# Kernel tuning notes

Hardware: AMD Instinct MI355X
Metric: run time of the kernel (lower is better)

The kernel has to match this reference:

```python
import jax, jax.numpy as jnp
import numpy as np

N = 100000   # number of nodes
D = 32       # uniform degree (CSR ptr = arange(N+1)*D)
B = 2048     # query batch size
F_IN, F_H, F_OUT = 64, 128, 64


def setup_inputs() -> dict:
    key = jax.random.key(0)
    ks = jax.random.split(key, 7)
    x = jax.random.normal(ks[0], (N, F_IN), dtype=jnp.float32)
    times = jax.random.uniform(ks[1], (B,), dtype=jnp.float32)
    ts = jax.random.uniform(ks[2], (N * D,), dtype=jnp.float32)
    W0 = jax.random.normal(ks[3], (F_IN, F_H), dtype=jnp.float32) / np.sqrt(F_IN)
    b0 = jnp.zeros((F_H,), dtype=jnp.float32)
    W1 = jax.random.normal(ks[4], (F_H, F_OUT), dtype=jnp.float32) / np.sqrt(F_H)
    b1 = jnp.zeros((F_OUT,), dtype=jnp.float32)
    batch = jax.random.randint(ks[5], (B,), 0, N, dtype=jnp.int64 if jax.config.jax_enable_x64 else jnp.int32)
    idx = jax.random.randint(ks[6], (N * D,), 0, N, dtype=jnp.int64 if jax.config.jax_enable_x64 else jnp.int32)
    return dict(x=x, times=times, ts=ts, W0=W0, b0=b0, W1=W1, b1=b1, batch=batch, idx=idx)


def reference(x, times, ts, W0, b0, W1, b1, batch, idx):
    # CSR with uniform degree D -> dense neighbor/timestamp matrices [N, D]
    idx_m = idx.reshape(N, D)
    ts_m = ts.reshape(N, D)

    # ---- layer-2 frontier: temporal neighbors of each query node + self loop
    nbrs1 = idx_m[batch]                      # [B, D]
    ts1 = ts_m[batch]                         # [B, D]
    mask1 = ts1 <= times[:, None]             # [B, D] edges with ts <= node time
    nodes = jnp.concatenate([nbrs1, batch[:, None]], axis=1)   # [B, D+1] (self appended)
    t2 = jnp.concatenate([ts1, times[:, None]], axis=1)        # [B, D+1] neighbor query times

    # ---- layer-1: for every frontier (node, time), temporal neighbors + self
    nbrs2 = idx_m[nodes]                      # [B, D+1, D]
    ts2 = ts_m[nodes]                         # [B, D+1, D]
    mask2 = ts2 <= t2[..., None]              # [B, D+1, D]

    # layer 0 embeddings are raw features; masked mean == scatter_mean with self loop
    h_nb = x[nbrs2]                           # [B, D+1, D, F_IN]  (dominant gather)
    agg0 = jnp.where(mask2[..., None], h_nb, 0.0).sum(axis=-2) + x[nodes]  # [B, D+1, F_IN]
    cnt0 = (mask2.sum(axis=-1) + 1).astype(x.dtype)[..., None]             # [B, D+1, 1]
    h1 = jax.nn.relu(agg0 / cnt0 @ W0 + b0)   # [B, D+1, F_H] = act(gcns[0](scatter_mean))

    # ---- layer-2 aggregation over (masked neighbors + self)
    mask_full = jnp.concatenate([mask1, jnp.ones((B, 1), dtype=bool)], axis=1)  # [B, D+1]
    agg1 = jnp.where(mask_full[..., None], h1, 0.0).sum(axis=1)                 # [B, F_H]
    cnt1 = mask_full.sum(axis=1).astype(x.dtype)[:, None]                       # [B, 1]
    out = jax.nn.relu(agg1 / cnt1 @ W1 + b1)  # [B, F_OUT] = act(gcns[1](scatter_mean))
    return out
```

## Files before the change

kernel.cpp:

```cpp
#include <hip/hip_runtime.h>

#define DEG   32
#define F_IN  64
#define F_H   128
#define F_OUT 64
#define NW    8
#define BLOCK (NW * 64)

__launch_bounds__(BLOCK, 4)
__global__ void flowgnn_kernel(const float* __restrict__ x,
                               const float* __restrict__ times,
                               const float* __restrict__ ts,
                               const float* __restrict__ W0,
                               const float* __restrict__ b0,
                               const float* __restrict__ W1,
                               const float* __restrict__ b1,
                               const int*   __restrict__ batch,
                               const int*   __restrict__ idx,
                               float*       __restrict__ out)
{
    __shared__ __align__(16) float W0s[F_IN * F_H];
    __shared__ float t2_s[DEG + 1];
    __shared__ int   nodes_s[DEG + 1];
    __shared__ __align__(16) float meanw[NW * F_IN];
    __shared__ __align__(16) float red[NW * F_H];
    __shared__ __align__(16) float aggm[F_H];

    const int b    = blockIdx.x;
    const int t    = threadIdx.x;
    const int wid  = t >> 6;
    const int lane = t & 63;

    const int   node0 = batch[b];
    const float tb    = times[b];

    {
        const float4* src = (const float4*)W0;
        float4*       dst = (float4*)W0s;
        #pragma unroll
        for (int i = t; i < (F_IN * F_H) / 4; i += BLOCK) dst[i] = src[i];
    }
    if (t < DEG) {
        t2_s[t]    = ts [node0 * DEG + t];
        nodes_s[t] = idx[node0 * DEG + t];
    }
    if (t == DEG) {
        t2_s[DEG]    = tb;
        nodes_s[DEG] = node0;
    }
    __syncthreads();

    const float b0x = b0[2 * lane];
    const float b0y = b0[2 * lane + 1];
    float a1x = 0.f, a1y = 0.f;

    for (int j = wid; j <= DEG; j += NW) {
        const float tq = t2_s[j];
        if (!(tq <= tb)) continue;

        const int node = nodes_s[j];
        const int l32  = lane & 31;
        const int   nb = idx[node * DEG + l32];
        const float tn = ts [node * DEG + l32];

        float acc = x[node * F_IN + lane];

        const unsigned long long bal = __ballot(tn <= tq);
        const unsigned ms = __builtin_amdgcn_readfirstlane((unsigned)(bal & 0xffffffffULL));
        const float cntf = (float)(__popc(ms) + 1);

        #pragma unroll
        for (int g = 0; g < 2; ++g) {
            float v[16];
            #pragma unroll
            for (int n = 0; n < 16; ++n) {
                v[n] = 0.f;
                const int r = g * 16 + n;
                if (ms & (1u << r)) {
                    const int nbr = __builtin_amdgcn_readlane(nb, r);
                    v[n] = x[nbr * F_IN + lane];
                }
            }
            #pragma unroll
            for (int n = 0; n < 16; ++n) acc += v[n];
        }
        const float mean = acc / cntf;

        meanw[wid * F_IN + lane] = mean;

        float hx = 0.f, hy = 0.f;
        #pragma unroll
        for (int f4 = 0; f4 < F_IN / 4; ++f4) {
            const float4 m4 = *(const float4*)&meanw[wid * F_IN + 4 * f4];
            const float2 wa = *(const float2*)&W0s[(4 * f4 + 0) * F_H + 2 * lane];
            const float2 wb = *(const float2*)&W0s[(4 * f4 + 1) * F_H + 2 * lane];
            const float2 wc = *(const float2*)&W0s[(4 * f4 + 2) * F_H + 2 * lane];
            const float2 wd = *(const float2*)&W0s[(4 * f4 + 3) * F_H + 2 * lane];
            hx += m4.x * wa.x; hy += m4.x * wa.y;
            hx += m4.y * wb.x; hy += m4.y * wb.y;
            hx += m4.z * wc.x; hy += m4.z * wc.y;
            hx += m4.w * wd.x; hy += m4.w * wd.y;
        }
        a1x += fmaxf(hx + b0x, 0.f);
        a1y += fmaxf(hy + b0y, 0.f);
    }

    red[wid * F_H + 2 * lane]     = a1x;
    red[wid * F_H + 2 * lane + 1] = a1y;
    __syncthreads();

    if (wid == 0) {
        bool mf = false;
        if (lane <= DEG) mf = (t2_s[lane] <= tb);
        const float cnt1 = (float)__popcll(__ballot(mf));

        float sx = 0.f, sy = 0.f;
        #pragma unroll
        for (int w = 0; w < NW; ++w) {
            sx += red[w * F_H + 2 * lane];
            sy += red[w * F_H + 2 * lane + 1];
        }
        aggm[2 * lane]     = sx / cnt1;
        aggm[2 * lane + 1] = sy / cnt1;

        float o = b1[lane];
        #pragma unroll
        for (int k4 = 0; k4 < F_H / 4; ++k4) {
            const float4 a4 = *(const float4*)&aggm[4 * k4];
            o += a4.x * W1[(4 * k4 + 0) * F_OUT + lane];
            o += a4.y * W1[(4 * k4 + 1) * F_OUT + lane];
            o += a4.z * W1[(4 * k4 + 2) * F_OUT + lane];
            o += a4.w * W1[(4 * k4 + 3) * F_OUT + lane];
        }
        out[b * F_OUT + lane] = fmaxf(o, 0.f);
    }
}

extern "C" void kernel_launch(void* const* d_in, const int* in_sizes, int n_in,
                              void* d_out, int out_size, void* d_ws, size_t ws_size,
                              hipStream_t stream)
{
    const float* x     = (const float*)d_in[0];
    const float* times = (const float*)d_in[1];
    const float* ts    = (const float*)d_in[2];
    const float* W0    = (const float*)d_in[3];
    const float* b0    = (const float*)d_in[4];
    const float* W1    = (const float*)d_in[5];
    const float* b1    = (const float*)d_in[6];
    const int*   batch = (const int*)d_in[7];
    const int*   idx   = (const int*)d_in[8];
    float*       out   = (float*)d_out;

    const int B = in_sizes[1];
    flowgnn_kernel<<<B, BLOCK, 0, stream>>>(x, times, ts, W0, b0, W1, b1, batch, idx, out);
}
```

Baseline: 133.5 us.

## Prefetch neighbor indices/masks into LDS and software-pipeline gathers with GEMM

```diff
diff --git a/kernel.cpp b/kernel.cpp
--- a/kernel.cpp
+++ b/kernel.cpp
@@ -7,7 +7,7 @@
 #define NW    8
 #define BLOCK (NW * 64)
 
-__launch_bounds__(BLOCK, 4)
+__launch_bounds__(BLOCK, 6)
 __global__ void flowgnn_kernel(const float* __restrict__ x,
                                const float* __restrict__ times,
                                const float* __restrict__ ts,
@@ -19,20 +19,31 @@
                                const int*   __restrict__ idx,
                                float*       __restrict__ out)
 {
-    __shared__ __align__(16) float W0s[F_IN * F_H];
-    __shared__ float t2_s[DEG + 1];
-    __shared__ int   nodes_s[DEG + 1];
-    __shared__ __align__(16) float meanw[NW * F_IN];
-    __shared__ __align__(16) float red[NW * F_H];
-    __shared__ __align__(16) float aggm[F_H];
+    __shared__ __align__(16) float smem[9868];
+    float*    W0s     = smem;
+    int*      idx_s   = (int*)(smem + 8192);
+    float*    t2_s    = smem + 9248;
+    int*      nodes_s = (int*)(smem + 9284);
+    unsigned* mask_s  = (unsigned*)(smem + 9320);
+    float*    meanw   = smem + 9356;
 
     const int b    = blockIdx.x;
     const int t    = threadIdx.x;
     const int wid  = t >> 6;
     const int lane = t & 63;
+    const int l32  = lane & 31;
+    const int hsel = (lane >> 5) << 4;
 
     const int   node0 = batch[b];
     const float tb    = times[b];
+    const float2* __restrict__ x2 = (const float2*)x;
+
+    if (t < DEG) {
+        t2_s[t]    = ts [node0 * DEG + t];
+        nodes_s[t] = idx[node0 * DEG + t];
+    }
+    if (t == DEG) { t2_s[DEG] = tb; nodes_s[DEG] = node0; }
+    __syncthreads();
 
     {
         const float4* src = (const float4*)W0;
@@ -40,54 +51,34 @@
         #pragma unroll
         for (int i = t; i < (F_IN * F_H) / 4; i += BLOCK) dst[i] = src[i];
     }
-    if (t < DEG) {
-        t2_s[t]    = ts [node0 * DEG + t];
-        nodes_s[t] = idx[node0 * DEG + t];
-    }
-    if (t == DEG) {
-        t2_s[DEG]    = tb;
-        nodes_s[DEG] = node0;
+    #pragma unroll
+    for (int q = 0; q < 3; ++q) {
+        const int p = t + q * BLOCK;
+        bool bit = false;
+        if (p < (DEG + 1) * DEG) {
+            const int j = p >> 5, d = p & 31;
+            const int nd = nodes_s[j];
+            idx_s[p] = idx[nd * DEG + d];
+            bit = (ts[nd * DEG + d] <= t2_s[j]);
+        }
+        const unsigned long long bal = __ballot(bit);
+        const int prow = (q * BLOCK + (t & ~63)) >> 5;
+        if (p < (DEG + 1) * DEG) {
+            if (lane == 0)  mask_s[prow]     = (unsigned)(bal & 0xffffffffULL);
+            if (lane == 32) mask_s[prow + 1] = (unsigned)(bal >> 32);
+        }
     }
     __syncthreads();
+
+    const unsigned long long liveM =
+        __ballot((lane <= DEG) ? (t2_s[lane] <= tb) : false);
 
     const float b0x = b0[2 * lane];
     const float b0y = b0[2 * lane + 1];
     float a1x = 0.f, a1y = 0.f;
+    int jprev = -1;
 
-    for (int j = wid; j <= DEG; j += NW) {
-        const float tq = t2_s[j];
-        if (!(tq <= tb)) continue;
-
-        const int node = nodes_s[j];
-        const int l32  = lane & 31;
-        const int   nb = idx[node * DEG + l32];
-        const float tn = ts [node * DEG + l32];
-
-        float acc = x[node * F_IN + lane];
-
-        const unsigned long long bal = __ballot(tn <= tq);
-        const unsigned ms = __builtin_amdgcn_readfirstlane((unsigned)(bal & 0xffffffffULL));
-        const float cntf = (float)(__popc(ms) + 1);
-
-        #pragma unroll
-        for (int g = 0; g < 2; ++g) {
-            float v[16];
-            #pragma unroll
-            for (int n = 0; n < 16; ++n) {
-                v[n] = 0.f;
-                const int r = g * 16 + n;
-                if (ms & (1u << r)) {
-                    const int nbr = __builtin_amdgcn_readlane(nb, r);
-                    v[n] = x[nbr * F_IN + lane];
-                }
-            }
-            #pragma unroll
-            for (int n = 0; n < 16; ++n) acc += v[n];
-        }
-        const float mean = acc / cntf;
-
-        meanw[wid * F_IN + lane] = mean;
-
+    auto do_gemm1 = [&]() {
         float hx = 0.f, hy = 0.f;
         #pragma unroll
         for (int f4 = 0; f4 < F_IN / 4; ++f4) {
@@ -103,17 +94,51 @@
         }
         a1x += fmaxf(hx + b0x, 0.f);
         a1y += fmaxf(hy + b0y, 0.f);
+    };
+
+    for (int j = wid; j <= DEG; j += NW) {
+        if (!((liveM >> j) & 1ULL)) continue;
+
+        const unsigned ms   = mask_s[j];
+        const int selfnode  = nodes_s[j];
+        const int* idr      = &idx_s[j * DEG];
+        float2 V[16];
+        #pragma unroll
+        for (int n = 0; n < 16; ++n) {
+            const int rid = idr[n + hsel];
+            V[n] = x2[rid * (F_IN / 2) + l32];
+        }
+        float2 sV = x2[selfnode * (F_IN / 2) + l32];
+
+        if (jprev >= 0) do_gemm1();
+
+        const unsigned msl = ms >> hsel;
+        float ax = 0.f, ay = 0.f;
+        #pragma unroll
+        for (int n = 0; n < 16; ++n) {
+            const bool k = (msl >> n) & 1u;
+            ax += k ? V[n].x : 0.f;
+            ay += k ? V[n].y : 0.f;
+        }
+        ax += __shfl_xor(ax, 32);
+        ay += __shfl_xor(ay, 32);
+        ax += sV.x; ay += sV.y;
+        const float rc = __builtin_amdgcn_rcpf((float)(__popc(ms) + 1));
+        if (lane < 32)
+            *(float2*)&meanw[wid * F_IN + 2 * l32] = make_float2(ax * rc, ay * rc);
+        jprev = j;
     }
+    if (jprev >= 0) do_gemm1();
 
+    __syncthreads();
+    float* red  = smem;
+    float* aggm = smem + NW * F_H;
     red[wid * F_H + 2 * lane]     = a1x;
     red[wid * F_H + 2 * lane + 1] = a1y;
     __syncthreads();
 
     if (wid == 0) {
-        bool mf = false;
-        if (lane <= DEG) mf = (t2_s[lane] <= tb);
-        const float cnt1 = (float)__popcll(__ballot(mf));
-
+        const float cnt1 = (float)__popcll(liveM);
         float sx = 0.f, sy = 0.f;
         #pragma unroll
         for (int w = 0; w < NW; ++w) {
```

New measurement: 141.4 us. 1.06x slower.
